# Kernel optimization log

Hardware: AMD Instinct MI355X
Metric: run time of the kernel (lower is better)

## Reference

```python
import jax, jax.numpy as jnp
import numpy as np
import math

DIM = 1024

def setup_inputs() -> dict:
    key = jax.random.key(0)
    ks = jax.random.split(key, 5)
    X = jax.random.normal(ks[0], (4, 2048, DIM), dtype=jnp.float32)
    # Linear params (stored as [in, out] so y = x @ W + b)
    W_in = jax.random.normal(ks[1], (DIM, 3 * DIM), dtype=jnp.float32) / math.sqrt(DIM)
    b_in = jnp.zeros((3 * DIM,), dtype=jnp.float32)
    W_out = jax.random.normal(ks[2], (DIM, DIM), dtype=jnp.float32) / math.sqrt(DIM)
    b_out = jnp.zeros((DIM,), dtype=jnp.float32)
    return {"X": X, "W_in": W_in, "b_in": b_in, "W_out": W_out, "b_out": b_out}

def reference(X, W_in, b_in, W_out, b_out):
    dim = X.shape[-1]
    QKV = X @ W_in + b_in                       # [B, S, 3*dim]
    Q, K, V = jnp.split(QKV, 3, axis=-1)        # each [B, S, dim]
    scores = jnp.einsum('bqd,bkd->bqk', Q, K) / math.sqrt(dim)  # [B, S, S]
    attn = jax.nn.softmax(scores, axis=-1)
    out = jnp.einsum('bqk,bkd->bqd', attn, V)   # [B, S, dim]
    return out @ W_out + b_out
```

## Files before the change

### kernel.cpp

```cpp
#include <hip/hip_runtime.h>
#include <hip/hip_bf16.h>
#include <math.h>

typedef __attribute__((ext_vector_type(8))) __bf16 bf16x8;
typedef __attribute__((ext_vector_type(4))) float f32x4;
typedef __attribute__((ext_vector_type(4))) unsigned int u32x4;

#define DIM 1024
#define SEQ 2048
#define BATCH 4
#define ROWS (BATCH*SEQ)

#define BAR() do { asm volatile("" ::: "memory"); __builtin_amdgcn_s_barrier(); asm volatile("" ::: "memory"); } while(0)
#define WAITV(n) asm volatile("s_waitcnt vmcnt(" #n ")" ::: "memory")
#define WAITL0() asm volatile("s_waitcnt lgkmcnt(0)" ::: "memory")
#define SCHED0() __builtin_amdgcn_sched_barrier(0)
#define PRIO(x) __builtin_amdgcn_s_setprio(x)

#define DSR(d, a, off) do { u32x4 _t; \
  asm volatile("ds_read_b128 %0, %1 offset:" #off : "=v"(_t) : "v"(a)); \
  (d) = __builtin_bit_cast(bf16x8, _t); } while(0)

__device__ __forceinline__ unsigned short f2bf(float f) {
  unsigned int u = __float_as_uint(f);
  u += 0x7FFF + ((u >> 16) & 1);
  return (unsigned short)(u >> 16);
}
__device__ __forceinline__ unsigned short to_bf_bits(float v) { return f2bf(v); }
__device__ __forceinline__ unsigned short to_bf_bits(unsigned short v) { return v; }

__device__ __forceinline__ void gload_lds16(const void* g, void* lds) {
  __builtin_amdgcn_global_load_lds((__attribute__((address_space(1))) void*)g,
                                   (__attribute__((address_space(3))) void*)lds,
                                   16, 0, 0);
}

__global__ __launch_bounds__(256)
void conv_f32_bf16(const float* __restrict__ src, unsigned short* __restrict__ dst, int n8) {
  int i = blockIdx.x * blockDim.x + threadIdx.x;
  if (i >= n8) return;
  const float4* s = reinterpret_cast<const float4*>(src) + (size_t)i * 2;
  float4 a = s[0], b = s[1];
  union { unsigned short h[8]; uint4 v; } p;
  p.h[0]=f2bf(a.x); p.h[1]=f2bf(a.y); p.h[2]=f2bf(a.z); p.h[3]=f2bf(a.w);
  p.h[4]=f2bf(b.x); p.h[5]=f2bf(b.y); p.h[6]=f2bf(b.z); p.h[7]=f2bf(b.w);
  reinterpret_cast<uint4*>(dst)[i] = p.v;
}

template<typename Tin>
__global__ __launch_bounds__(1024)
void transpose_conv(const Tin* __restrict__ src, int ldsrc, size_t sstride,
                    unsigned short* __restrict__ dst, int lddst, size_t dstride) {
  __shared__ unsigned short tile[32][33];
  const Tin* s = src + (size_t)blockIdx.z * sstride;
  unsigned short* d = dst + (size_t)blockIdx.z * dstride;
  int tx = threadIdx.x, ty = threadIdx.y;
  int r = blockIdx.y * 32 + ty, c = blockIdx.x * 32 + tx;
  tile[ty][tx] = to_bf_bits(s[(size_t)r * ldsrc + c]);
  __syncthreads();
  d[(size_t)(blockIdx.x * 32 + ty) * lddst + blockIdx.y * 32 + tx] = tile[tx][ty];
}

#define EPI_QKV 0
#define EPI_F32 1
#define EPI_BF16 2
#define EPI_BIAS_F32 3

template<int BN, int EPI>
__global__ __launch_bounds__(512, 2)
void gemm8(const unsigned short* __restrict__ A, int lda, size_t sA,
           const unsigned short* __restrict__ B, int ldb, size_t sB,
           void* __restrict__ C, int ldc, size_t sC,
           const float* __restrict__ bias, int K) {
  constexpr int NREP = BN / 64;
  constexpr int NW = 16 * NREP;
  __shared__ unsigned short As[2 * 256 * 64];
  __shared__ unsigned short Bs[2 * BN * 64];

  const int tid = threadIdx.x;
  const int lane = tid & 63, wave = tid >> 6;
  const int wm = wave >> 2, wn = wave & 3;
  const int fr = lane & 15, fk = lane >> 4;
  const int tileM = blockIdx.y * 256, tileN = blockIdx.x * BN;
  const unsigned short* Ab = A + (size_t)blockIdx.z * sA;
  const unsigned short* Bb = B + (size_t)blockIdx.z * sB;

  const int srow = tid >> 3;
  const int sg = (tid & 7) ^ (srow & 7);

  auto stageA = [&](int buf, int half, int k0) {
#pragma unroll
    for (int q = 0; q < 2; ++q) {
      int rl = half * 128 + q * 64 + srow;
      gload_lds16(Ab + (size_t)(tileM + rl) * lda + k0 + sg * 8,
                  &As[buf * (256 * 64) + (half * 128 + q * 64) * 64 + tid * 8]);
    }
  };
  auto stageB = [&](int buf, int part, int k0) {
#pragma unroll
    for (int q = 0; q < 2; ++q) {
      int rl = part * 128 + q * 64 + srow;
      gload_lds16(Bb + (size_t)(tileN + rl) * ldb + k0 + sg * 8,
                  &Bs[buf * (BN * 64) + (part * 128 + q * 64) * 64 + tid * 8]);
    }
  };

  f32x4 acc[8][NREP];
#pragma unroll
  for (int m = 0; m < 8; ++m)
#pragma unroll
    for (int n = 0; n < NREP; ++n) acc[m][n] = (f32x4){0.f, 0.f, 0.f, 0.f};

  const int NS = K >> 6;
  const unsigned asb = (unsigned)(size_t)(__attribute__((address_space(3))) unsigned short*)As;
  const unsigned bsb = (unsigned)(size_t)(__attribute__((address_space(3))) unsigned short*)Bs;
  const unsigned aoff = (unsigned)((wm * 128 + fr) * 128 + ((fk ^ (fr & 7)) << 4));
  const unsigned boff = (unsigned)((wn * NW + fr) * 128 + ((fk ^ (fr & 7)) << 4));

  stageA(0, 0, 0); stageA(0, 1, 0); stageB(0, 0, 0);
  if (BN == 256) stageB(0, 1, 0);
  if (NS > 1) { stageA(1, 0, 64); WAITV(2); } else { WAITV(0); }
  BAR();

  bf16x8 afLo[4][2], afHi[4][2], bg[NREP][2];

  for (int t = 0; t < NS; ++t) {
    const unsigned aA0 = asb + ((t & 1) ? 32768u : 0u) + aoff;
    const unsigned aA1 = aA0 ^ 64u;
    const unsigned bB0 = bsb + ((t & 1) ? (unsigned)(BN * 128) : 0u) + boff;
    const unsigned bB1 = bB0 ^ 64u;
    const int k1 = (t + 1) << 6, k2 = (t + 2) << 6;
    const int nb = (t & 1) ^ 1;

    if constexpr (BN == 256) {
      DSR(afLo[0][0], aA0, 0); DSR(afLo[1][0], aA0, 2048); DSR(afLo[2][0], aA0, 4096); DSR(afLo[3][0], aA0, 6144);
      DSR(afLo[0][1], aA1, 0); DSR(afLo[1][1], aA1, 2048); DSR(afLo[2][1], aA1, 4096); DSR(afLo[3][1], aA1, 6144);
      DSR(bg[0][0], bB0, 0); DSR(bg[1][0], bB0, 2048);
      DSR(bg[0][1], bB1, 0); DSR(bg[1][1], bB1, 2048);
      if (t + 1 < NS) stageA(nb, 1, k1);
      BAR(); WAITL0(); SCHED0();
      PRIO(1);
#pragma unroll
      for (int kk = 0; kk < 2; ++kk)
#pragma unroll
        for (int m = 0; m < 4; ++m)
#pragma unroll
          for (int n = 0; n < 2; ++n)
            acc[m][n] = __builtin_amdgcn_mfma_f32_16x16x32_bf16(afLo[m][kk], bg[n][kk], acc[m][n], 0, 0, 0);
      PRIO(0); SCHED0();
      BAR();
      DSR(bg[2][0], bB0, 4096); DSR(bg[3][0], bB0, 6144);
      DSR(bg[2][1], bB1, 4096); DSR(bg[3][1], bB1, 6144);
      if (t + 1 < NS) stageB(nb, 0, k1);
      BAR(); WAITL0(); SCHED0();
      PRIO(1);
#pragma unroll
      for (int kk = 0; kk < 2; ++kk)
#pragma unroll
        for (int m = 0; m < 4; ++m)
#pragma unroll
          for (int n = 0; n < 2; ++n)
            acc[m][2 + n] = __builtin_amdgcn_mfma_f32_16x16x32_bf16(afLo[m][kk], bg[2 + n][kk], acc[m][2 + n], 0, 0, 0);
      PRIO(0); SCHED0();
      BAR();
      DSR(afHi[0][0], aA0, 8192); DSR(afHi[1][0], aA0, 10240); DSR(afHi[2][0], aA0, 12288); DSR(afHi[3][0], aA0, 14336);
      DSR(afHi[0][1], aA1, 8192); DSR(afHi[1][1], aA1, 10240); DSR(afHi[2][1], aA1, 12288); DSR(afHi[3][1], aA1, 14336);
      if (t + 1 < NS) stageB(nb, 1, k1);
      BAR(); WAITL0(); SCHED0();
      PRIO(1);
#pragma unroll
      for (int kk = 0; kk < 2; ++kk)
#pragma unroll
        for (int m = 0; m < 4; ++m)
#pragma unroll
          for (int n = 0; n < 2; ++n)
            acc[4 + m][n] = __builtin_amdgcn_mfma_f32_16x16x32_bf16(afHi[m][kk], bg[n][kk], acc[4 + m][n], 0, 0, 0);
      PRIO(0); SCHED0();
      BAR();
      if (t + 2 < NS) stageA(t & 1, 0, k2);
      BAR();
      PRIO(1);
#pragma unroll
      for (int kk = 0; kk < 2; ++kk)
#pragma unroll
        for (int m = 0; m < 4; ++m)
#pragma unroll
          for (int n = 0; n < 2; ++n)
            acc[4 + m][2 + n] = __builtin_amdgcn_mfma_f32_16x16x32_bf16(afHi[m][kk], bg[2 + n][kk], acc[4 + m][2 + n], 0, 0, 0);
      PRIO(0); SCHED0();
      if (t + 1 < NS) { if (t + 2 < NS) { WAITV(2); } else { WAITV(0); } }
      BAR();
    } else {
      DSR(afLo[0][0], aA0, 0); DSR(afLo[1][0], aA0, 2048); DSR(afLo[2][0], aA0, 4096); DSR(afLo[3][0], aA0, 6144);
      DSR(afLo[0][1], aA1, 0); DSR(afLo[1][1], aA1, 2048); DSR(afLo[2][1], aA1, 4096); DSR(afLo[3][1], aA1, 6144);
      DSR(bg[0][0], bB0, 0); DSR(bg[1][0], bB0, 2048);
      DSR(bg[0][1], bB1, 0); DSR(bg[1][1], bB1, 2048);
      if (t + 1 < NS) { stageA(nb, 1, k1); stageB(nb, 0, k1); }
      BAR(); WAITL0(); SCHED0();
      PRIO(1);
#pragma unroll
      for (int kk = 0; kk < 2; ++kk)
#pragma unroll
        for (int m = 0; m < 4; ++m)
#pragma unroll
          for (int n = 0; n < 2; ++n)
            acc[m][n] = __builtin_amdgcn_mfma_f32_16x16x32_bf16(afLo[m][kk], bg[n][kk], acc[m][n], 0, 0, 0);
      PRIO(0); SCHED0();
      BAR();
      DSR(afHi[0][0], aA0, 8192); DSR(afHi[1][0], aA0, 10240); DSR(afHi[2][0], aA0, 12288); DSR(afHi[3][0], aA0, 14336);
      DSR(afHi[0][1], aA1, 8192); DSR(afHi[1][1], aA1, 10240); DSR(afHi[2][1], aA1, 12288); DSR(afHi[3][1], aA1, 14336);
      if (t + 2 < NS) stageA(t & 1, 0, k2);
      BAR(); WAITL0(); SCHED0();
      PRIO(1);
#pragma unroll
      for (int kk = 0; kk < 2; ++kk)
#pragma unroll
        for (int m = 0; m < 4; ++m)
#pragma unroll
          for (int n = 0; n < 2; ++n)
            acc[4 + m][n] = __builtin_amdgcn_mfma_f32_16x16x32_bf16(afHi[m][kk], bg[n][kk], acc[4 + m][n], 0, 0, 0);
      PRIO(0); SCHED0();
      if (t + 1 < NS) { if (t + 2 < NS) { WAITV(2); } else { WAITV(0); } }
      BAR();
    }
  }

#pragma unroll
  for (int m = 0; m < 8; ++m)
#pragma unroll
    for (int n = 0; n < NREP; ++n)
#pragma unroll
      for (int j = 0; j < 4; ++j) {
        int row = tileM + wm * 128 + m * 16 + fk * 4 + j;
        int col = tileN + wn * NW + n * 16 + fr;
        float v = acc[m][n][j];
        if (EPI == EPI_QKV) {
          v += bias[col];
          if (col < DIM) v *= 0.03125f;
          ((unsigned short*)C + (size_t)blockIdx.z * sC)[(size_t)row * ldc + col] = f2bf(v);
        } else if (EPI == EPI_BF16) {
          ((unsigned short*)C + (size_t)blockIdx.z * sC)[(size_t)row * ldc + col] = f2bf(v);
        } else if (EPI == EPI_BIAS_F32) {
          ((float*)C + (size_t)blockIdx.z * sC)[(size_t)row * ldc + col] = v + bias[col];
        } else {
          ((float*)C + (size_t)blockIdx.z * sC)[(size_t)row * ldc + col] = v;
        }
      }
}

__global__ __launch_bounds__(256)
void softmax_kernel(float* __restrict__ S, size_t zstride) {
  __shared__ float red[8];
  float* row = S + (size_t)blockIdx.y * zstride + (size_t)blockIdx.x * SEQ;
  const int tid = threadIdx.x;
  const int lane = tid & 63, wave = tid >> 6;
  const float4* src = reinterpret_cast<const float4*>(row) + tid * 2;
  float4 a = src[0], b = src[1];
  float v[8] = {a.x, a.y, a.z, a.w, b.x, b.y, b.z, b.w};
  float m = v[0];
#pragma unroll
  for (int i = 1; i < 8; ++i) m = fmaxf(m, v[i]);
  for (int o = 32; o; o >>= 1) m = fmaxf(m, __shfl_xor(m, o));
  if (lane == 0) red[wave] = m;
  __syncthreads();
  m = fmaxf(fmaxf(red[0], red[1]), fmaxf(red[2], red[3]));
  float e[8], s = 0.f;
#pragma unroll
  for (int i = 0; i < 8; ++i) { e[i] = expf(v[i] - m); s += e[i]; }
  for (int o = 32; o; o >>= 1) s += __shfl_xor(s, o);
  if (lane == 0) red[4 + wave] = s;
  __syncthreads();
  s = red[4] + red[5] + red[6] + red[7];
  float inv = 1.f / s;
  union { unsigned short h[8]; uint4 u; } p;
#pragma unroll
  for (int i = 0; i < 8; ++i) p.h[i] = f2bf(e[i] * inv);
  reinterpret_cast<uint4*>(row)[tid] = p.u;
}

extern "C" void kernel_launch(void* const* d_in, const int* in_sizes, int n_in,
                              void* d_out, int out_size, void* d_ws, size_t ws_size,
                              hipStream_t stream) {
  const float* X     = (const float*)d_in[0];
  const float* W_in  = (const float*)d_in[1];
  const float* b_in  = (const float*)d_in[2];
  const float* W_out = (const float*)d_in[3];
  const float* b_out = (const float*)d_in[4];
  float* out = (float*)d_out;
  char* ws = (char*)d_ws;

  size_t o = 0;
  auto alloc = [&](size_t bytes) { size_t r = o; o += (bytes + 255) & ~(size_t)255; return r; };
  unsigned short* Xbf   = (unsigned short*)(ws + alloc((size_t)ROWS * DIM * 2));
  unsigned short* WinT  = (unsigned short*)(ws + alloc((size_t)3 * DIM * DIM * 2));
  unsigned short* WoutT = (unsigned short*)(ws + alloc((size_t)DIM * DIM * 2));
  unsigned short* QKV   = (unsigned short*)(ws + alloc((size_t)ROWS * 3 * DIM * 2));
  size_t fixed = o;
  size_t per_batch = (((size_t)SEQ * SEQ * 4 + 255) & ~(size_t)255) +
                     (((size_t)DIM * SEQ * 2 + 255) & ~(size_t)255);
  int G = (ws_size >= fixed + 4 * per_batch) ? BATCH : 1;
  float*          Sc = (float*)(ws + alloc((size_t)G * SEQ * SEQ * 4));
  unsigned short* Vt = (unsigned short*)(ws + alloc((size_t)G * DIM * SEQ * 2));
  unsigned short* O  = Xbf;

  conv_f32_bf16<<<(ROWS * DIM / 8 + 255) / 256, 256, 0, stream>>>(X, Xbf, ROWS * DIM / 8);
  transpose_conv<float><<<dim3(3 * DIM / 32, DIM / 32, 1), dim3(32, 32), 0, stream>>>(
      W_in, 3 * DIM, 0, WinT, DIM, 0);
  transpose_conv<float><<<dim3(DIM / 32, DIM / 32, 1), dim3(32, 32), 0, stream>>>(
      W_out, DIM, 0, WoutT, DIM, 0);
  gemm8<128, EPI_QKV><<<dim3(3 * DIM / 128, ROWS / 256, 1), 512, 0, stream>>>(
      Xbf, DIM, 0, WinT, DIM, 0, QKV, 3 * DIM, 0, b_in, DIM);

  for (int b0 = 0; b0 < BATCH; b0 += G) {
    const unsigned short* Qb = QKV + (size_t)b0 * SEQ * 3 * DIM;
    const unsigned short* Kb = Qb + DIM;
    const unsigned short* Vb = Qb + 2 * DIM;
    transpose_conv<unsigned short><<<dim3(DIM / 32, SEQ / 32, G), dim3(32, 32), 0, stream>>>(
        Vb, 3 * DIM, (size_t)SEQ * 3 * DIM, Vt, SEQ, (size_t)DIM * SEQ);
    gemm8<256, EPI_F32><<<dim3(SEQ / 256, SEQ / 256, G), 512, 0, stream>>>(
        Qb, 3 * DIM, (size_t)SEQ * 3 * DIM, Kb, 3 * DIM, (size_t)SEQ * 3 * DIM,
        Sc, SEQ, (size_t)SEQ * SEQ, nullptr, DIM);
    softmax_kernel<<<dim3(SEQ, G), 256, 0, stream>>>(Sc, (size_t)SEQ * SEQ);
    gemm8<128, EPI_BF16><<<dim3(DIM / 128, SEQ / 256, G), 512, 0, stream>>>(
        (const unsigned short*)Sc, 2 * SEQ, (size_t)2 * SEQ * SEQ,
        Vt, SEQ, (size_t)DIM * SEQ,
        O + (size_t)b0 * SEQ * DIM, DIM, (size_t)SEQ * DIM, nullptr, SEQ);
  }
  gemm8<128, EPI_BIAS_F32><<<dim3(DIM / 128, ROWS / 256, 1), 512, 0, stream>>>(
      O, DIM, 0, WoutT, DIM, 0, out, DIM, 0, b_out, DIM);
}
```

Baseline: 230.4 us.

## Restructure GEMM prefetch schedule to stage B two tiles ahead and widen QKV tile

The GEMM main loop is re-pipelined. A tiles are now prefetched one stage ahead, and B tiles two stages ahead into the current buffer. B fragments are split into two register groups, and in the BN=128 path MFMA work is divided into finer k-halves interleaved with the loads. The QKV projection switches to 256-wide N tiles, which halves the grid and increases per-block reuse. This trades more in-flight loads and registers, and fewer blocks, for hiding global-load latency better.

New measurement: 229.5 us. No clear change (-0.4%).

```diff
diff --git a/kernel.cpp b/kernel.cpp
--- a/kernel.cpp
+++ b/kernel.cpp
@@ -93,15 +93,15 @@
     for (int q = 0; q < 2; ++q) {
       int rl = half * 128 + q * 64 + srow;
       gload_lds16(Ab + (size_t)(tileM + rl) * lda + k0 + sg * 8,
-                  &As[buf * (256 * 64) + (half * 128 + q * 64) * 64 + tid * 8]);
+                  &As[buf * (256 * 64) + rl * 64 + (tid & 7) * 8]);
     }
   };
-  auto stageB = [&](int buf, int part, int k0) {
+  auto stageB = [&](int buf, int half, int k0) {
 #pragma unroll
     for (int q = 0; q < 2; ++q) {
-      int rl = part * 128 + q * 64 + srow;
+      int rl = half * 128 + q * 64 + srow;
       gload_lds16(Bb + (size_t)(tileN + rl) * ldb + k0 + sg * 8,
-                  &Bs[buf * (BN * 64) + (part * 128 + q * 64) * 64 + tid * 8]);
+                  &Bs[buf * (BN * 64) + rl * 64 + (tid & 7) * 8]);
     }
   };
 
@@ -117,27 +117,44 @@
   const unsigned aoff = (unsigned)((wm * 128 + fr) * 128 + ((fk ^ (fr & 7)) << 4));
   const unsigned boff = (unsigned)((wn * NW + fr) * 128 + ((fk ^ (fr & 7)) << 4));
 
-  stageA(0, 0, 0); stageA(0, 1, 0); stageB(0, 0, 0);
-  if (BN == 256) stageB(0, 1, 0);
-  if (NS > 1) { stageA(1, 0, 64); WAITV(2); } else { WAITV(0); }
+  if constexpr (BN == 256) {
+    stageB(0, 0, 0); stageB(0, 1, 0); stageA(0, 0, 0); stageA(0, 1, 0);
+    if (NS > 1) { stageB(1, 0, 64); stageB(1, 1, 64); WAITV(4); } else { WAITV(0); }
+  } else {
+    stageB(0, 0, 0); stageA(0, 0, 0); stageA(0, 1, 0);
+    if (NS > 1) { stageB(1, 0, 64); WAITV(2); } else { WAITV(0); }
+  }
   BAR();
 
-  bf16x8 afLo[4][2], afHi[4][2], bg[NREP][2];
+  bf16x8 afLo[4][2], afHi[4][2], bgA[2][2], bgB[2][2];
 
   for (int t = 0; t < NS; ++t) {
-    const unsigned aA0 = asb + ((t & 1) ? 32768u : 0u) + aoff;
-    const unsigned aA1 = aA0 ^ 64u;
-    const unsigned bB0 = bsb + ((t & 1) ? (unsigned)(BN * 128) : 0u) + boff;
-    const unsigned bB1 = bB0 ^ 64u;
+    const int cb = t & 1, nb = cb ^ 1;
+    const unsigned aA0 = asb + (unsigned)cb * 32768u + aoff, aA1 = aA0 ^ 64u;
+    const unsigned bB0 = bsb + (unsigned)cb * (unsigned)(BN * 128) + boff, bB1 = bB0 ^ 64u;
     const int k1 = (t + 1) << 6, k2 = (t + 2) << 6;
-    const int nb = (t & 1) ^ 1;
 
     if constexpr (BN == 256) {
       DSR(afLo[0][0], aA0, 0); DSR(afLo[1][0], aA0, 2048); DSR(afLo[2][0], aA0, 4096); DSR(afLo[3][0], aA0, 6144);
       DSR(afLo[0][1], aA1, 0); DSR(afLo[1][1], aA1, 2048); DSR(afLo[2][1], aA1, 4096); DSR(afLo[3][1], aA1, 6144);
-      DSR(bg[0][0], bB0, 0); DSR(bg[1][0], bB0, 2048);
-      DSR(bg[0][1], bB1, 0); DSR(bg[1][1], bB1, 2048);
+      DSR(bgA[0][0], bB0, 0); DSR(bgA[1][0], bB0, 2048);
+      DSR(bgA[0][1], bB1, 0); DSR(bgA[1][1], bB1, 2048);
+      if (t + 1 < NS) stageA(nb, 0, k1);
+      BAR(); WAITL0(); SCHED0();
+      PRIO(1);
+#pragma unroll
+      for (int kk = 0; kk < 2; ++kk)
+#pragma unroll
+        for (int m = 0; m < 4; ++m)
+#pragma unroll
+          for (int n = 0; n < 2; ++n)
+            acc[m][n] = __builtin_amdgcn_mfma_f32_16x16x32_bf16(afLo[m][kk], bgA[n][kk], acc[m][n], 0, 0, 0);
+      PRIO(0); SCHED0();
+      BAR();
+      DSR(bgB[0][0], bB0, 4096); DSR(bgB[1][0], bB0, 6144);
+      DSR(bgB[0][1], bB1, 4096); DSR(bgB[1][1], bB1, 6144);
       if (t + 1 < NS) stageA(nb, 1, k1);
+      if (t + 2 < NS) stageB(cb, 0, k2);
       BAR(); WAITL0(); SCHED0();
       PRIO(1);
 #pragma unroll
@@ -146,26 +163,12 @@
         for (int m = 0; m < 4; ++m)
 #pragma unroll
           for (int n = 0; n < 2; ++n)
-            acc[m][n] = __builtin_amdgcn_mfma_f32_16x16x32_bf16(afLo[m][kk], bg[n][kk], acc[m][n], 0, 0, 0);
-      PRIO(0); SCHED0();
-      BAR();
-      DSR(bg[2][0], bB0, 4096); DSR(bg[3][0], bB0, 6144);
-      DSR(bg[2][1], bB1, 4096); DSR(bg[3][1], bB1, 6144);
-      if (t + 1 < NS) stageB(nb, 0, k1);
-      BAR(); WAITL0(); SCHED0();
-      PRIO(1);
-#pragma unroll
-      for (int kk = 0; kk < 2; ++kk)
-#pragma unroll
-        for (int m = 0; m < 4; ++m)
-#pragma unroll
-          for (int n = 0; n < 2; ++n)
-            acc[m][2 + n] = __builtin_amdgcn_mfma_f32_16x16x32_bf16(afLo[m][kk], bg[2 + n][kk], acc[m][2 + n], 0, 0, 0);
+            acc[m][2 + n] = __builtin_amdgcn_mfma_f32_16x16x32_bf16(afLo[m][kk], bgB[n][kk], acc[m][2 + n], 0, 0, 0);
       PRIO(0); SCHED0();
       BAR();
       DSR(afHi[0][0], aA0, 8192); DSR(afHi[1][0], aA0, 10240); DSR(afHi[2][0], aA0, 12288); DSR(afHi[3][0], aA0, 14336);
       DSR(afHi[0][1], aA1, 8192); DSR(afHi[1][1], aA1, 10240); DSR(afHi[2][1], aA1, 12288); DSR(afHi[3][1], aA1, 14336);
-      if (t + 1 < NS) stageB(nb, 1, k1);
+      if (t + 2 < NS) stageB(cb, 1, k2);
       BAR(); WAITL0(); SCHED0();
       PRIO(1);
 #pragma unroll
@@ -174,10 +177,8 @@
         for (int m = 0; m < 4; ++m)
 #pragma unroll
           for (int n = 0; n < 2; ++n)
-            acc[4 + m][n] = __builtin_amdgcn_mfma_f32_16x16x32_bf16(afHi[m][kk], bg[n][kk], acc[4 + m][n], 0, 0, 0);
-      PRIO(0); SCHED0();
-      BAR();
-      if (t + 2 < NS) stageA(t & 1, 0, k2);
+            acc[4 + m][n] = __builtin_amdgcn_mfma_f32_16x16x32_bf16(afHi[m][kk], bgA[n][kk], acc[4 + m][n], 0, 0, 0);
+      PRIO(0); SCHED0();
       BAR();
       PRIO(1);
 #pragma unroll
@@ -186,39 +187,53 @@
         for (int m = 0; m < 4; ++m)
 #pragma unroll
           for (int n = 0; n < 2; ++n)
-            acc[4 + m][2 + n] = __builtin_amdgcn_mfma_f32_16x16x32_bf16(afHi[m][kk], bg[2 + n][kk], acc[4 + m][2 + n], 0, 0, 0);
-      PRIO(0); SCHED0();
-      if (t + 1 < NS) { if (t + 2 < NS) { WAITV(2); } else { WAITV(0); } }
+            acc[4 + m][2 + n] = __builtin_amdgcn_mfma_f32_16x16x32_bf16(afHi[m][kk], bgB[n][kk], acc[4 + m][2 + n], 0, 0, 0);
+      PRIO(0); SCHED0();
+      if (t + 1 < NS) { if (t + 2 < NS) { WAITV(4); } else { WAITV(0); } }
       BAR();
     } else {
       DSR(afLo[0][0], aA0, 0); DSR(afLo[1][0], aA0, 2048); DSR(afLo[2][0], aA0, 4096); DSR(afLo[3][0], aA0, 6144);
+      DSR(bgA[0][0], bB0, 0); DSR(bgA[1][0], bB0, 2048);
+      if (t + 1 < NS) stageA(nb, 0, k1);
+      BAR(); WAITL0(); SCHED0();
+      PRIO(1);
+#pragma unroll
+      for (int m = 0; m < 4; ++m)
+#pragma unroll
+        for (int n = 0; n < 2; ++n)
+          acc[m][n] = __builtin_amdgcn_mfma_f32_16x16x32_bf16(afLo[m][0], bgA[n][0], acc[m][n], 0, 0, 0);
+      PRIO(0); SCHED0();
+      BAR();
       DSR(afLo[0][1], aA1, 0); DSR(afLo[1][1], aA1, 2048); DSR(afLo[2][1], aA1, 4096); DSR(afLo[3][1], aA1, 6144);
-      DSR(bg[0][0], bB0, 0); DSR(bg[1][0], bB0, 2048);
-      DSR(bg[0][1], bB1, 0); DSR(bg[1][1], bB1, 2048);
-      if (t + 1 < NS) { stageA(nb, 1, k1); stageB(nb, 0, k1); }
-      BAR(); WAITL0(); SCHED0();
-      PRIO(1);
-#pragma unroll
-      for (int kk = 0; kk < 2; ++kk)
-#pragma unroll
-        for (int m = 0; m < 4; ++m)
-#pragma unroll
-          for (int n = 0; n < 2; ++n)
-            acc[m][n] = __builtin_amdgcn_mfma_f32_16x16x32_bf16(afLo[m][kk], bg[n][kk], acc[m][n], 0, 0, 0);
+      DSR(bgA[0][1], bB1, 0); DSR(bgA[1][1], bB1, 2048);
+      if (t + 1 < NS) stageA(nb, 1, k1);
+      BAR(); WAITL0(); SCHED0();
+      PRIO(1);
+#pragma unroll
+      for (int m = 0; m < 4; ++m)
+#pragma unroll
+        for (int n = 0; n < 2; ++n)
+          acc[m][n] = __builtin_amdgcn_mfma_f32_16x16x32_bf16(afLo[m][1], bgA[n][1], acc[m][n], 0, 0, 0);
       PRIO(0); SCHED0();
       BAR();
       DSR(afHi[0][0], aA0, 8192); DSR(afHi[1][0], aA0, 10240); DSR(afHi[2][0], aA0, 12288); DSR(afHi[3][0], aA0, 14336);
       DSR(afHi[0][1], aA1, 8192); DSR(afHi[1][1], aA1, 10240); DSR(afHi[2][1], aA1, 12288); DSR(afHi[3][1], aA1, 14336);
-      if (t + 2 < NS) stageA(t & 1, 0, k2);
-      BAR(); WAITL0(); SCHED0();
-      PRIO(1);
-#pragma unroll
-      for (int kk = 0; kk < 2; ++kk)
-#pragma unroll
-        for (int m = 0; m < 4; ++m)
-#pragma unroll
-          for (int n = 0; n < 2; ++n)
-            acc[4 + m][n] = __builtin_amdgcn_mfma_f32_16x16x32_bf16(afHi[m][kk], bg[n][kk], acc[4 + m][n], 0, 0, 0);
+      if (t + 2 < NS) stageB(cb, 0, k2);
+      BAR(); WAITL0(); SCHED0();
+      PRIO(1);
+#pragma unroll
+      for (int m = 0; m < 4; ++m)
+#pragma unroll
+        for (int n = 0; n < 2; ++n)
+          acc[4 + m][n] = __builtin_amdgcn_mfma_f32_16x16x32_bf16(afHi[m][0], bgA[n][0], acc[4 + m][n], 0, 0, 0);
+      PRIO(0); SCHED0();
+      BAR();
+      PRIO(1);
+#pragma unroll
+      for (int m = 0; m < 4; ++m)
+#pragma unroll
+        for (int n = 0; n < 2; ++n)
+          acc[4 + m][n] = __builtin_amdgcn_mfma_f32_16x16x32_bf16(afHi[m][1], bgA[n][1], acc[4 + m][n], 0, 0, 0);
       PRIO(0); SCHED0();
       if (t + 1 < NS) { if (t + 2 < NS) { WAITV(2); } else { WAITV(0); } }
       BAR();
@@ -308,7 +323,7 @@
       W_in, 3 * DIM, 0, WinT, DIM, 0);
   transpose_conv<float><<<dim3(DIM / 32, DIM / 32, 1), dim3(32, 32), 0, stream>>>(
       W_out, DIM, 0, WoutT, DIM, 0);
-  gemm8<128, EPI_QKV><<<dim3(3 * DIM / 128, ROWS / 256, 1), 512, 0, stream>>>(
+  gemm8<256, EPI_QKV><<<dim3(3 * DIM / 256, ROWS / 256, 1), 512, 0, stream>>>(
       Xbf, DIM, 0, WinT, DIM, 0, QKV, 3 * DIM, 0, b_in, DIM);
 
   for (int b0 = 0; b0 < BATCH; b0 += G) {
```
